# Kernel tuning notes

Hardware: AMD Instinct MI355X
Metric: run time of the kernel (lower is better)

The kernel has to match this reference:

```python
import jax, jax.numpy as jnp
import numpy as np

NUM_GRAPHS = 64
NODE_SZ = 200
FEAT = 200
HID = 256          # hidden_size; each signed branch outputs HID//2
HALF = HID // 2
N_NODES = NUM_GRAPHS * NODE_SZ
N_EDGES = 409600
NUM_LAYERS = 3


def _lin_init(key, out_f, in_f):
    kw, kb = jax.random.split(key)
    s = 1.0 / np.sqrt(in_f)
    W = jax.random.uniform(kw, (out_f, in_f), minval=-s, maxval=s, dtype=jnp.float32)
    b = jax.random.uniform(kb, (out_f,), minval=-s, maxval=s, dtype=jnp.float32)
    return W, b


def setup_inputs() -> dict:
    key = jax.random.key(0)
    ks = jax.random.split(key, 16)
    x = jax.random.normal(ks[0], (N_NODES, FEAT), dtype=jnp.float32)
    edge_index = jax.random.randint(ks[1], (2, N_EDGES), 0, N_NODES, dtype=jnp.int64)
    edge_weight = jax.random.normal(ks[2], (N_EDGES,), dtype=jnp.float32)
    batch = jnp.repeat(jnp.arange(NUM_GRAPHS, dtype=jnp.int64), NODE_SZ)

    # signed conv layer params: layer0 in=FEAT, layers 1..: in=HID; each lin maps 2*in -> HALF
    Wp0, bp0 = _lin_init(ks[3], HALF, 2 * FEAT)
    Wn0, bn0 = _lin_init(ks[4], HALF, 2 * FEAT)
    Wp1, bp1 = _lin_init(ks[5], HALF, 2 * HID)
    Wn1, bn1 = _lin_init(ks[6], HALF, 2 * HID)
    Wp2, bp2 = _lin_init(ks[7], HALF, 2 * HID)
    Wn2, bn2 = _lin_init(ks[8], HALF, 2 * HID)
    Wr, br = _lin_init(ks[9], HID, NODE_SZ * HID)   # readout_lin
    Wl, bl = _lin_init(ks[10], 1, HID)              # final lin
    return dict(x=x, edge_index=edge_index, edge_weight=edge_weight, batch=batch,
                Wp0=Wp0, bp0=bp0, Wn0=Wn0, bn0=bn0,
                Wp1=Wp1, bp1=bp1, Wn1=Wn1, bn1=bn1,
                Wp2=Wp2, bp2=bp2, Wn2=Wn2, bn2=bn2,
                Wr=Wr, br=br, Wl=Wl, bl=bl)


def _signed_conv(x, src, dst, w, Wp, bp, Wn, bn):
    # edge-weighted signed mean aggregation, split by weight sign
    xs = x[src]                                   # [E, D] gather
    pw = jnp.where(w > 0, w, 0.0)
    nw = jnp.where(w < 0, -w, 0.0)
    agg_p = jax.ops.segment_sum(pw[:, None] * xs, dst, num_segments=N_NODES)
    agg_n = jax.ops.segment_sum(nw[:, None] * xs, dst, num_segments=N_NODES)
    deg_p = jax.ops.segment_sum((w > 0).astype(x.dtype), dst, num_segments=N_NODES)
    deg_n = jax.ops.segment_sum((w < 0).astype(x.dtype), dst, num_segments=N_NODES)
    agg_p = agg_p / jnp.maximum(deg_p, 1.0)[:, None]
    agg_n = agg_n / jnp.maximum(deg_n, 1.0)[:, None]
    hp = jnp.concatenate([agg_p, x], -1) @ Wp.T + bp
    hn = jnp.concatenate([agg_n, x], -1) @ Wn.T + bn
    return jnp.concatenate([hp, hn], -1)          # [N, HID]


def reference(x, edge_index, edge_weight, batch,
              Wp0, bp0, Wn0, bn0, Wp1, bp1, Wn1, bn1, Wp2, bp2, Wn2, bn2,
              Wr, br, Wl, bl):
    src, dst = edge_index[0], edge_index[1]
    convs = [(Wp0, bp0, Wn0, bn0), (Wp1, bp1, Wn1, bn1), (Wp2, bp2, Wn2, bn2)]
    h = x
    for i, (Wp, bp, Wn, bn) in enumerate(convs):
        h = _signed_conv(h, src, dst, edge_weight, Wp, bp, Wn, bn)
        if i < NUM_LAYERS - 1:
            h = jax.nn.leaky_relu(h, negative_slope=0.01)
    # per-graph readout: batch is contiguous with NODE_SZ nodes per graph,
    # so the boolean-mask+view loop is exactly a reshape.
    g = h.reshape(NUM_GRAPHS, NODE_SZ * HID)
    g = g @ Wr.T + br                             # [G, HID]
    # dropout(p=0.5) is identity in eval mode
    return g @ Wl.T + bl                          # [G, 1]
```

## Files before the change

### kernel.cpp

```cpp
#include <hip/hip_runtime.h>

#define NUM_GRAPHS 64
#define NODE_SZ    200
#define FEAT       200
#define HID        256
#define HALF       128
#define N_NODES    (NUM_GRAPHS * NODE_SZ)
#define KREAD      (NODE_SZ * HID)
#define HBLK       128

typedef unsigned short ushort_t;
typedef unsigned int uint_t;
typedef __attribute__((ext_vector_type(8))) short bf16x8;
typedef __attribute__((ext_vector_type(4))) float f32x4;

#define GAS(p) ((const __attribute__((address_space(1))) void*)(p))
#define LAS(p) ((__attribute__((address_space(3))) void*)(p))

__device__ __forceinline__ float bf2f(ushort_t u) {
    union { unsigned int i; float f; } v; v.i = ((unsigned int)u) << 16; return v.f;
}
__device__ __forceinline__ ushort_t f2bf(float f) {
    union { float f; unsigned int i; } v; v.f = f;
    unsigned int x = v.i;
    unsigned int r = (x + 0x7fffu + ((x >> 16) & 1u)) >> 16;
    return (ushort_t)r;
}

__global__ __launch_bounds__(1024) void bhist_kernel(const int* __restrict__ ei,
                                                     const float* __restrict__ ew,
                                                     uint_t* __restrict__ bh, int E) {
    __shared__ uint_t h[N_NODES];
    for (int i = threadIdx.x; i < N_NODES; i += 1024) h[i] = 0;
    __syncthreads();
    int b = blockIdx.x;
    int epb = (E + HBLK - 1) / HBLK;
    int e0 = b * epb, e1 = min(e0 + epb, E);
    for (int e = e0 + threadIdx.x; e < e1; e += 1024) {
        int dst = ei[E + e];
        float w = ew[e];
        if (w > 0.0f)      atomicAdd(&h[dst], 1u);
        else if (w < 0.0f) atomicAdd(&h[dst], 0x10000u);
    }
    __syncthreads();
    uint_t* out = bh + (size_t)b * N_NODES;
    for (int i = threadIdx.x * 4; i < N_NODES; i += 4096)
        *(uint4*)&out[i] = *(const uint4*)&h[i];
}

__global__ void colpref_kernel(uint_t* __restrict__ bh, int* __restrict__ counts,
                               int* __restrict__ cnt_p) {
    int n = blockIdx.x * 256 + threadIdx.x;
    if (n >= N_NODES) return;
    uint_t seq = 0;
#pragma unroll 1
    for (int b = 0; b < HBLK; b += 8) {
        uint_t v[8];
#pragma unroll
        for (int j = 0; j < 8; ++j) v[j] = bh[(size_t)(b + j) * N_NODES + n];
#pragma unroll
        for (int j = 0; j < 8; ++j) {
            bh[(size_t)(b + j) * N_NODES + n] = seq;
            seq += v[j];
        }
    }
    counts[n] = (int)((seq & 0xffffu) + (seq >> 16));
    cnt_p[n]  = (int)(seq & 0xffffu);
}

__global__ __launch_bounds__(1024) void scan_kernel(const int* __restrict__ counts,
                                                    const int* __restrict__ cnt_p,
                                                    uint2* __restrict__ obnd, int n) {
    const int PER = 13;
    int t = threadIdx.x;
    int start = t * PER;
    int local[PER];
    int sum = 0;
#pragma unroll
    for (int i = 0; i < PER; ++i) {
        int idx = start + i;
        int v = (idx < n) ? counts[idx] : 0;
        local[i] = sum;
        sum += v;
    }
    int lane = t & 63, wid = t >> 6;
    int inc = sum;
#pragma unroll
    for (int d = 1; d < 64; d <<= 1) {
        int up = __shfl_up(inc, d);
        if (lane >= d) inc += up;
    }
    __shared__ int wsum[16], woff[16];
    if (lane == 63) wsum[wid] = inc;
    __syncthreads();
    if (t < 16) {
        int acc = 0;
        for (int j = 0; j < 16; ++j) if (j < t) acc += wsum[j];
        woff[t] = acc;
    }
    __syncthreads();
    int base = woff[wid] + (inc - sum);
#pragma unroll
    for (int i = 0; i < PER; ++i) {
        int idx = start + i;
        if (idx < n) {
            uint_t off = (uint_t)(base + local[i]);
            obnd[idx] = make_uint2(off, off + (uint_t)cnt_p[idx]);
        }
    }
    if (t == 1023) {
        uint_t tot = (uint_t)(base + sum);
        obnd[n] = make_uint2(tot, tot);
    }
}

__global__ __launch_bounds__(1024) void scat_prep_kernel(
        const int* __restrict__ ei, const float* __restrict__ ew,
        const uint_t* __restrict__ bh, const uint2* __restrict__ obnd,
        uint2* __restrict__ es, int E,
        const float* __restrict__ W0p, const float* __restrict__ W0n,
        const float* __restrict__ W1p, const float* __restrict__ W1n,
        const float* __restrict__ W2p, const float* __restrict__ W2n,
        const float* __restrict__ x,
        ushort_t* __restrict__ wall, ushort_t* __restrict__ xb) {
    __shared__ uint_t cur[N_NODES];
    int bx = blockIdx.x;
    if (bx < HBLK) {
        const uint_t* pref = bh + (size_t)bx * N_NODES;
        for (int i = threadIdx.x * 4; i < N_NODES; i += 4096)
            *(uint4*)&cur[i] = *(const uint4*)&pref[i];
        __syncthreads();
        int epb = (E + HBLK - 1) / HBLK;
        int e0 = bx * epb, e1 = min(e0 + epb, E);
        for (int e = e0 + threadIdx.x; e < e1; e += 1024) {
            int src = ei[e];
            int dst = ei[E + e];
            float w = ew[e];
            if (w > 0.0f) {
                uint_t old = atomicAdd(&cur[dst], 1u);
                uint_t pos = obnd[dst].x + (old & 0xffffu);
                es[pos] = make_uint2((uint_t)src, __float_as_uint(w));
            } else if (w < 0.0f) {
                uint_t old = atomicAdd(&cur[dst], 0x10000u);
                uint_t pos = obnd[dst].y + (old >> 16);
                es[pos] = make_uint2((uint_t)src, __float_as_uint(-w));
            }
        }
    } else if (bx < 512) {
        int idx = (bx - 128) * 1024 + threadIdx.x;
        int layer = idx >> 17;
        int within = idx & 131071;
        int rr = within >> 8;
        int col = within & 255;
        const float* Wp = (layer == 0) ? W0p : (layer == 1) ? W1p : W2p;
        const float* Wn = (layer == 0) ? W0n : (layer == 1) ? W1n : W2n;
        int Ks = (layer == 0) ? 200 : 256;
        int q = rr >> 7;
        const float* Wsrc = (q & 1) ? Wn : Wp;
        int row = rr & 127;
        int scol = col + ((q >> 1) ? Ks : 0);
        float v = (col < Ks) ? Wsrc[(size_t)row * (2 * Ks) + scol] : 0.0f;
        wall[idx] = f2bf(v);
    } else {
        int idx = (bx - 512) * 1024 + threadIdx.x;
        int n = idx >> 6;
        int c0 = (idx & 63) * 4;
        ushort4 o = {0, 0, 0, 0};
        if (c0 < 200) {
            float4 v = *(const float4*)&x[(size_t)n * 200 + c0];
            o.x = f2bf(v.x); o.y = f2bf(v.y); o.z = f2bf(v.z); o.w = f2bf(v.w);
        }
        *(ushort4*)&xb[(size_t)n * 256 + c0] = o;
    }
}

template <int KSTEPS>
__global__ __launch_bounds__(256) void gemm_mfma(
        const ushort_t* __restrict__ A,
        const ushort_t* __restrict__ B,
        ushort_t* __restrict__ Y) {
    __shared__ __align__(16) ushort_t As[2][32 * 32];
    __shared__ __align__(16) ushort_t Bs[2][128 * 32];
    int mBase = blockIdx.x * 32;
    int nBase = blockIdx.y * 128;
    int tid  = threadIdx.x;
    int lane = tid & 63;
    int wv   = tid >> 6;
    int r    = lane & 15;
    int quad = lane >> 4;

    int rowA = tid >> 2, colA = (tid & 3) * 8;
    const ushort_t* gA  = A + (size_t)(mBase + (rowA & 31)) * 256 + colA;
    const ushort_t* gB0 = B + (size_t)(nBase + rowA) * 256 + colA;
    const ushort_t* gB1 = B + (size_t)(nBase + rowA + 64) * 256 + colA;

    f32x4 acc00 = {0.f,0.f,0.f,0.f}, acc01 = {0.f,0.f,0.f,0.f};
    f32x4 acc10 = {0.f,0.f,0.f,0.f}, acc11 = {0.f,0.f,0.f,0.f};

    if (tid < 128)
        __builtin_amdgcn_global_load_lds(GAS(gA), LAS(&As[0][wv * 512]), 16, 0, 0);
    __builtin_amdgcn_global_load_lds(GAS(gB0), LAS(&Bs[0][wv * 512]), 16, 0, 0);
    __builtin_amdgcn_global_load_lds(GAS(gB1), LAS(&Bs[0][2048 + wv * 512]), 16, 0, 0);

    for (int kt = 0; kt < KSTEPS; ++kt) {
        int cur = kt & 1;
        __syncthreads();
        if (kt + 1 < KSTEPS) {
            int kB = (kt + 1) * 32;
            if (tid < 128)
                __builtin_amdgcn_global_load_lds(GAS(gA + kB), LAS(&As[cur ^ 1][wv * 512]), 16, 0, 0);
            __builtin_amdgcn_global_load_lds(GAS(gB0 + kB), LAS(&Bs[cur ^ 1][wv * 512]), 16, 0, 0);
            __builtin_amdgcn_global_load_lds(GAS(gB1 + kB), LAS(&Bs[cur ^ 1][2048 + wv * 512]), 16, 0, 0);
        }
        bf16x8 a0 = *(const bf16x8*)&As[cur][r * 32 + quad * 8];
        bf16x8 a1 = *(const bf16x8*)&As[cur][(16 + r) * 32 + quad * 8];
        bf16x8 b0 = *(const bf16x8*)&Bs[cur][(wv * 32 + r) * 32 + quad * 8];
        bf16x8 b1 = *(const bf16x8*)&Bs[cur][(wv * 32 + 16 + r) * 32 + quad * 8];
        acc00 = __builtin_amdgcn_mfma_f32_16x16x32_bf16(a0, b0, acc00, 0, 0, 0);
        acc01 = __builtin_amdgcn_mfma_f32_16x16x32_bf16(a0, b1, acc01, 0, 0, 0);
        acc10 = __builtin_amdgcn_mfma_f32_16x16x32_bf16(a1, b0, acc10, 0, 0, 0);
        acc11 = __builtin_amdgcn_mfma_f32_16x16x32_bf16(a1, b1, acc11, 0, 0, 0);
    }
#pragma unroll
    for (int jn = 0; jn < 2; ++jn) {
        int cl = nBase + wv * 32 + jn * 16 + r;
        f32x4 am0 = jn ? acc01 : acc00;
        f32x4 am1 = jn ? acc11 : acc10;
#pragma unroll
        for (int reg = 0; reg < 4; ++reg) {
            int m0 = mBase + quad * 4 + reg;
            Y[(size_t)m0 * 512 + cl]        = f2bf(am0[reg]);
            Y[(size_t)(m0 + 16) * 512 + cl] = f2bf(am1[reg]);
        }
    }
}

template <bool LEAKY>
__global__ __launch_bounds__(256) void aggcomb_kernel(
        const ushort_t* __restrict__ Y,
        const uint2* __restrict__ obnd,
        const uint2* __restrict__ es,
        const float* __restrict__ bp, const float* __restrict__ bn,
        ushort_t* __restrict__ out) {
    int lane = threadIdx.x & 63;
    int wv   = threadIdx.x >> 6;
    int n = blockIdx.x * 4 + wv;
    int c0 = lane * 2;
    uint2 ob = obnd[n];
    uint_t off = ob.x, mid = ob.y, end = obnd[n + 1].x;

    float accp[2] = {0.f, 0.f};
    float accn[2] = {0.f, 0.f};

#pragma unroll 1
    for (int phase = 0; phase < 2; ++phase) {
        uint_t lo = phase ? mid : off;
        uint_t hi = phase ? end : mid;
        float* acc = phase ? accn : accp;
        const ushort_t* Yb = Y + (phase ? 128 : 0) + c0;
#pragma unroll 1
        for (uint_t base = lo; base < hi; base += 64) {
            int cnt = (int)min(64u, hi - base);
            uint2 rec = es[base + (uint_t)min(lane, cnt - 1)];
            int i = 0;
#pragma unroll 1
            for (; i + 8 <= cnt; i += 8) {
                int s[8]; float w[8]; uint_t u[8];
#pragma unroll
                for (int j = 0; j < 8; ++j) {
                    s[j] = __shfl((int)rec.x, i + j);
                    w[j] = __uint_as_float((uint_t)__shfl((int)rec.y, i + j));
                }
#pragma unroll
                for (int j = 0; j < 8; ++j) u[j] = *(const uint_t*)&Yb[(size_t)s[j] * 512];
#pragma unroll
                for (int j = 0; j < 8; ++j) {
                    acc[0] = fmaf(w[j], bf2f((ushort_t)(u[j] & 0xffffu)), acc[0]);
                    acc[1] = fmaf(w[j], bf2f((ushort_t)(u[j] >> 16)), acc[1]);
                }
            }
#pragma unroll 1
            for (; i < cnt; ++i) {
                int s = __shfl((int)rec.x, i);
                float w = __uint_as_float((uint_t)__shfl((int)rec.y, i));
                uint_t u = *(const uint_t*)&Yb[(size_t)s * 512];
                acc[0] = fmaf(w, bf2f((ushort_t)(u & 0xffffu)), acc[0]);
                acc[1] = fmaf(w, bf2f((ushort_t)(u >> 16)), acc[1]);
            }
        }
    }

    float dp = fmaxf((float)(mid - off), 1.0f);
    float dn = fmaxf((float)(end - mid), 1.0f);
    float rp = 1.0f / dp, rn = 1.0f / dn;
    uint_t zp = *(const uint_t*)&Y[(size_t)n * 512 + 256 + c0];
    uint_t zn = *(const uint_t*)&Y[(size_t)n * 512 + 384 + c0];
    float vp0 = fmaf(accp[0], rp, bf2f((ushort_t)(zp & 0xffffu)) + bp[c0]);
    float vp1 = fmaf(accp[1], rp, bf2f((ushort_t)(zp >> 16))     + bp[c0 + 1]);
    float vn0 = fmaf(accn[0], rn, bf2f((ushort_t)(zn & 0xffffu)) + bn[c0]);
    float vn1 = fmaf(accn[1], rn, bf2f((ushort_t)(zn >> 16))     + bn[c0 + 1]);
    if (LEAKY) {
        vp0 = (vp0 > 0.0f) ? vp0 : 0.01f * vp0;
        vp1 = (vp1 > 0.0f) ? vp1 : 0.01f * vp1;
        vn0 = (vn0 > 0.0f) ? vn0 : 0.01f * vn0;
        vn1 = (vn1 > 0.0f) ? vn1 : 0.01f * vn1;
    }
    uint_t op = (uint_t)f2bf(vp0) | ((uint_t)f2bf(vp1) << 16);
    uint_t on = (uint_t)f2bf(vn0) | ((uint_t)f2bf(vn1) << 16);
    *(uint_t*)&out[(size_t)n * 256 + c0]       = op;
    *(uint_t*)&out[(size_t)n * 256 + 128 + c0] = on;
}

__global__ __launch_bounds__(256) void readout_mfma(
        const ushort_t* __restrict__ h, const float* __restrict__ Wr,
        float* __restrict__ partial) {
    __shared__ __align__(16) ushort_t As[64 * 32];
    __shared__ __align__(16) ushort_t Bs[64 * 32];
    int nBase  = blockIdx.x * 64;
    int kStart = blockIdx.y * 800;
    int tid  = threadIdx.x;
    int lane = tid & 63;
    int wv   = tid >> 6;
    int r    = lane & 15;
    int quad = lane >> 4;

    f32x4 acc[4];
#pragma unroll
    for (int j = 0; j < 4; ++j) acc[j] = (f32x4){0.f, 0.f, 0.f, 0.f};

    for (int kt = 0; kt < 25; ++kt) {
        int kBase = kStart + kt * 32;
        int lin = tid * 8;
        int row = lin >> 5, col = lin & 31;
        *(uint4*)&As[lin] = *(const uint4*)&h[(size_t)row * KREAD + kBase + col];
        {
            const float* wp = &Wr[(size_t)(nBase + row) * KREAD + kBase + col];
            float4 f0 = *(const float4*)&wp[0];
            float4 f1 = *(const float4*)&wp[4];
            ushort4 b0, b1;
            b0.x = f2bf(f0.x); b0.y = f2bf(f0.y); b0.z = f2bf(f0.z); b0.w = f2bf(f0.w);
            b1.x = f2bf(f1.x); b1.y = f2bf(f1.y); b1.z = f2bf(f1.z); b1.w = f2bf(f1.w);
            *(ushort4*)&Bs[lin]     = b0;
            *(ushort4*)&Bs[lin + 4] = b1;
        }
        __syncthreads();
        bf16x8 a = *(const bf16x8*)&As[(wv * 16 + r) * 32 + quad * 8];
#pragma unroll
        for (int j = 0; j < 4; ++j) {
            bf16x8 b = *(const bf16x8*)&Bs[(j * 16 + r) * 32 + quad * 8];
            acc[j] = __builtin_amdgcn_mfma_f32_16x16x32_bf16(a, b, acc[j], 0, 0, 0);
        }
        __syncthreads();
    }
    float* out = partial + (size_t)blockIdx.y * (64 * HID);
#pragma unroll
    for (int j = 0; j < 4; ++j) {
        int c = nBase + j * 16 + r;
#pragma unroll
        for (int reg = 0; reg < 4; ++reg) {
            int g = wv * 16 + quad * 4 + reg;
            out[g * HID + c] = acc[j][reg];
        }
    }
}

__global__ void final_kernel(const float* __restrict__ partial, const float* __restrict__ br,
                             const float* __restrict__ Wl, const float* __restrict__ bl,
                             float* __restrict__ out) {
    int g = blockIdx.x;
    int c = threadIdx.x;
    float s = 0.0f;
#pragma unroll 4
    for (int k = 0; k < 64; ++k) s += partial[(size_t)k * (64 * HID) + g * HID + c];
    float v = (s + br[c]) * Wl[c];
#pragma unroll
    for (int d = 32; d > 0; d >>= 1) v += __shfl_down(v, d);
    __shared__ float sh[4];
    if ((c & 63) == 0) sh[c >> 6] = v;
    __syncthreads();
    if (c == 0) out[g] = sh[0] + sh[1] + sh[2] + sh[3] + bl[0];
}

extern "C" void kernel_launch(void* const* d_in, const int* in_sizes, int n_in,
                              void* d_out, int out_size, void* d_ws, size_t ws_size,
                              hipStream_t stream) {
    const float* x  = (const float*)d_in[0];
    const int*   ei = (const int*)d_in[1];
    const float* ew = (const float*)d_in[2];
    const float* Wp0 = (const float*)d_in[4];
    const float* bp0 = (const float*)d_in[5];
    const float* Wn0 = (const float*)d_in[6];
    const float* bn0 = (const float*)d_in[7];
    const float* Wp1 = (const float*)d_in[8];
    const float* bp1 = (const float*)d_in[9];
    const float* Wn1 = (const float*)d_in[10];
    const float* bn1 = (const float*)d_in[11];
    const float* Wp2 = (const float*)d_in[12];
    const float* bp2 = (const float*)d_in[13];
    const float* Wn2 = (const float*)d_in[14];
    const float* bn2 = (const float*)d_in[15];
    const float* Wr  = (const float*)d_in[16];
    const float* br  = (const float*)d_in[17];
    const float* Wl  = (const float*)d_in[18];
    const float* bl  = (const float*)d_in[19];
    const int E = in_sizes[1] / 2;

    char* ws = (char*)d_ws;
    float*    partial = (float*)(ws + 0);
    uint_t*   bh      = (uint_t*)(ws + 4194304);
    int*      counts  = (int*)(ws + 10747904);
    int*      cnt_p   = (int*)(ws + 10799104);
    uint2*    obnd    = (uint2*)(ws + 10850304);
    uint2*    es      = (uint2*)(ws + 10952768);
    ushort_t* Yall    = (ushort_t*)(ws + 14229568);
    ushort_t* hA      = (ushort_t*)(ws + 27336768);
    ushort_t* hB      = (ushort_t*)(ws + 33890368);
    ushort_t* wall    = (ushort_t*)(ws + 40443968);
    ushort_t* xb      = (ushort_t*)(ws + 41230400);

    hipLaunchKernelGGL(bhist_kernel, dim3(HBLK), dim3(1024), 0, stream, ei, ew, bh, E);
    hipLaunchKernelGGL(colpref_kernel, dim3((N_NODES + 255) / 256), dim3(256), 0, stream,
                       bh, counts, cnt_p);
    hipLaunchKernelGGL(scan_kernel, dim3(1), dim3(1024), 0, stream, counts, cnt_p, obnd, N_NODES);
    hipLaunchKernelGGL(scat_prep_kernel, dim3(1312), dim3(1024), 0, stream,
                       ei, ew, bh, obnd, es, E,
                       Wp0, Wn0, Wp1, Wn1, Wp2, Wn2, x, wall, xb);

    hipLaunchKernelGGL((gemm_mfma<7>), dim3(N_NODES / 32, 4), dim3(256), 0, stream,
                       xb, wall + 0 * 131072, Yall);
    hipLaunchKernelGGL((aggcomb_kernel<true>), dim3(N_NODES / 4), dim3(256), 0, stream,
                       Yall, obnd, es, bp0, bn0, hA);
    hipLaunchKernelGGL((gemm_mfma<8>), dim3(N_NODES / 32, 4), dim3(256), 0, stream,
                       hA, wall + 1 * 131072, Yall);
    hipLaunchKernelGGL((aggcomb_kernel<true>), dim3(N_NODES / 4), dim3(256), 0, stream,
                       Yall, obnd, es, bp1, bn1, hB);
    hipLaunchKernelGGL((gemm_mfma<8>), dim3(N_NODES / 32, 4), dim3(256), 0, stream,
                       hB, wall + 2 * 131072, Yall);
    hipLaunchKernelGGL((aggcomb_kernel<false>), dim3(N_NODES / 4), dim3(256), 0, stream,
                       Yall, obnd, es, bp2, bn2, hA);

    hipLaunchKernelGGL(readout_mfma, dim3(4, 64), dim3(256), 0, stream, hA, Wr, partial);
    hipLaunchKernelGGL(final_kernel, dim3(NUM_GRAPHS), dim3(256), 0, stream,
                       partial, br, Wl, bl, (float*)d_out);
}
```

Baseline: 296.8 us.

## Fuse edge scatter with first GEMM, use global-atomic histogram, enlarge GEMM tiles

The per-block LDS histogram, column prefix kernel and large per-block offset buffer are replaced by one global-atomic histogram over packed positive/negative counts, which the scan reads directly. The CSR edge scatter now runs in the same launch as the layer-0 GEMM: the first blocks do the GEMM and the rest place edges. Weight/x conversion and counter zeroing move into a separate prep kernel. The GEMM switches to 128x256 tiles with 512 threads, always doing 8 K-steps. This cuts kernel launches and offset traffic, at the cost of more contention on global atomics and a non-deterministic edge order within each node.

```diff
diff --git a/kernel.cpp b/kernel.cpp
--- a/kernel.cpp
+++ b/kernel.cpp
@@ -7,7 +7,6 @@
 #define HALF       128
 #define N_NODES    (NUM_GRAPHS * NODE_SZ)
 #define KREAD      (NODE_SZ * HID)
-#define HBLK       128
 
 typedef unsigned short ushort_t;
 typedef unsigned int uint_t;
@@ -27,59 +26,66 @@
     return (ushort_t)r;
 }
 
-__global__ __launch_bounds__(1024) void bhist_kernel(const int* __restrict__ ei,
-                                                     const float* __restrict__ ew,
-                                                     uint_t* __restrict__ bh, int E) {
-    __shared__ uint_t h[N_NODES];
-    for (int i = threadIdx.x; i < N_NODES; i += 1024) h[i] = 0;
-    __syncthreads();
-    int b = blockIdx.x;
-    int epb = (E + HBLK - 1) / HBLK;
-    int e0 = b * epb, e1 = min(e0 + epb, E);
-    for (int e = e0 + threadIdx.x; e < e1; e += 1024) {
+__global__ __launch_bounds__(256) void prep_kernel(
+        const float* __restrict__ Wp0, const float* __restrict__ Wn0,
+        const float* __restrict__ Wp1, const float* __restrict__ Wn1,
+        const float* __restrict__ Wp2, const float* __restrict__ Wn2,
+        const float* __restrict__ x,
+        uint_t* __restrict__ cntcur, ushort_t* __restrict__ wall,
+        ushort_t* __restrict__ xb) {
+    int gid = blockIdx.x * 256 + threadIdx.x;
+    const int GS = gridDim.x * 256;
+    for (int i = gid; i < 2 * N_NODES; i += GS) cntcur[i] = 0u;
+    for (int idx = gid; idx < 3 * 131072; idx += GS) {
+        int layer = idx >> 17, within = idx & 131071;
+        int rr = within >> 8, col = within & 255;
+        const float* Wp = (layer == 0) ? Wp0 : (layer == 1) ? Wp1 : Wp2;
+        const float* Wn = (layer == 0) ? Wn0 : (layer == 1) ? Wn1 : Wn2;
+        int Ks = (layer == 0) ? 200 : 256;
+        int q = rr >> 7;
+        const float* Wsrc = (q & 1) ? Wn : Wp;
+        int row = rr & 127;
+        int scol = col + ((q >> 1) ? Ks : 0);
+        float v = (col < Ks) ? Wsrc[(size_t)row * (2 * Ks) + scol] : 0.0f;
+        wall[idx] = f2bf(v);
+    }
+    for (int idx = gid; idx < N_NODES * 64; idx += GS) {
+        int n = idx >> 6, c0 = (idx & 63) * 4;
+        ushort4 o = {0, 0, 0, 0};
+        if (c0 < 200) {
+            float4 v = *(const float4*)&x[(size_t)n * 200 + c0];
+            o.x = f2bf(v.x); o.y = f2bf(v.y); o.z = f2bf(v.z); o.w = f2bf(v.w);
+        }
+        *(ushort4*)&xb[(size_t)n * 256 + c0] = o;
+    }
+}
+
+__global__ __launch_bounds__(512) void hist_kernel(const int* __restrict__ ei,
+                                                   const float* __restrict__ ew,
+                                                   uint_t* __restrict__ cnt, int E) {
+    int e = blockIdx.x * 512 + threadIdx.x;
+    if (e < E) {
         int dst = ei[E + e];
         float w = ew[e];
-        if (w > 0.0f)      atomicAdd(&h[dst], 1u);
-        else if (w < 0.0f) atomicAdd(&h[dst], 0x10000u);
-    }
-    __syncthreads();
-    uint_t* out = bh + (size_t)b * N_NODES;
-    for (int i = threadIdx.x * 4; i < N_NODES; i += 4096)
-        *(uint4*)&out[i] = *(const uint4*)&h[i];
-}
-
-__global__ void colpref_kernel(uint_t* __restrict__ bh, int* __restrict__ counts,
-                               int* __restrict__ cnt_p) {
-    int n = blockIdx.x * 256 + threadIdx.x;
-    if (n >= N_NODES) return;
-    uint_t seq = 0;
-#pragma unroll 1
-    for (int b = 0; b < HBLK; b += 8) {
-        uint_t v[8];
-#pragma unroll
-        for (int j = 0; j < 8; ++j) v[j] = bh[(size_t)(b + j) * N_NODES + n];
-#pragma unroll
-        for (int j = 0; j < 8; ++j) {
-            bh[(size_t)(b + j) * N_NODES + n] = seq;
-            seq += v[j];
-        }
-    }
-    counts[n] = (int)((seq & 0xffffu) + (seq >> 16));
-    cnt_p[n]  = (int)(seq & 0xffffu);
-}
-
-__global__ __launch_bounds__(1024) void scan_kernel(const int* __restrict__ counts,
-                                                    const int* __restrict__ cnt_p,
+        if (w > 0.0f)      atomicAdd(&cnt[dst], 1u);
+        else if (w < 0.0f) atomicAdd(&cnt[dst], 0x10000u);
+    }
+}
+
+__global__ __launch_bounds__(1024) void scan_kernel(const uint_t* __restrict__ cnt,
                                                     uint2* __restrict__ obnd, int n) {
     const int PER = 13;
     int t = threadIdx.x;
     int start = t * PER;
     int local[PER];
+    uint_t pcnt[PER];
     int sum = 0;
 #pragma unroll
     for (int i = 0; i < PER; ++i) {
         int idx = start + i;
-        int v = (idx < n) ? counts[idx] : 0;
+        uint_t c = (idx < n) ? cnt[idx] : 0u;
+        int v = (int)((c & 0xffffu) + (c >> 16));
+        pcnt[i] = c & 0xffffu;
         local[i] = sum;
         sum += v;
     }
@@ -105,7 +111,7 @@
         int idx = start + i;
         if (idx < n) {
             uint_t off = (uint_t)(base + local[i]);
-            obnd[idx] = make_uint2(off, off + (uint_t)cnt_p[idx]);
+            obnd[idx] = make_uint2(off, off + pcnt[i]);
         }
     }
     if (t == 1023) {
@@ -114,134 +120,111 @@
     }
 }
 
-__global__ __launch_bounds__(1024) void scat_prep_kernel(
-        const int* __restrict__ ei, const float* __restrict__ ew,
-        const uint_t* __restrict__ bh, const uint2* __restrict__ obnd,
-        uint2* __restrict__ es, int E,
-        const float* __restrict__ W0p, const float* __restrict__ W0n,
-        const float* __restrict__ W1p, const float* __restrict__ W1n,
-        const float* __restrict__ W2p, const float* __restrict__ W2n,
-        const float* __restrict__ x,
-        ushort_t* __restrict__ wall, ushort_t* __restrict__ xb) {
-    __shared__ uint_t cur[N_NODES];
-    int bx = blockIdx.x;
-    if (bx < HBLK) {
-        const uint_t* pref = bh + (size_t)bx * N_NODES;
-        for (int i = threadIdx.x * 4; i < N_NODES; i += 4096)
-            *(uint4*)&cur[i] = *(const uint4*)&pref[i];
-        __syncthreads();
-        int epb = (E + HBLK - 1) / HBLK;
-        int e0 = bx * epb, e1 = min(e0 + epb, E);
-        for (int e = e0 + threadIdx.x; e < e1; e += 1024) {
-            int src = ei[e];
-            int dst = ei[E + e];
-            float w = ew[e];
-            if (w > 0.0f) {
-                uint_t old = atomicAdd(&cur[dst], 1u);
-                uint_t pos = obnd[dst].x + (old & 0xffffu);
-                es[pos] = make_uint2((uint_t)src, __float_as_uint(w));
-            } else if (w < 0.0f) {
-                uint_t old = atomicAdd(&cur[dst], 0x10000u);
-                uint_t pos = obnd[dst].y + (old >> 16);
-                es[pos] = make_uint2((uint_t)src, __float_as_uint(-w));
-            }
-        }
-    } else if (bx < 512) {
-        int idx = (bx - 128) * 1024 + threadIdx.x;
-        int layer = idx >> 17;
-        int within = idx & 131071;
-        int rr = within >> 8;
-        int col = within & 255;
-        const float* Wp = (layer == 0) ? W0p : (layer == 1) ? W1p : W2p;
-        const float* Wn = (layer == 0) ? W0n : (layer == 1) ? W1n : W2n;
-        int Ks = (layer == 0) ? 200 : 256;
-        int q = rr >> 7;
-        const float* Wsrc = (q & 1) ? Wn : Wp;
-        int row = rr & 127;
-        int scol = col + ((q >> 1) ? Ks : 0);
-        float v = (col < Ks) ? Wsrc[(size_t)row * (2 * Ks) + scol] : 0.0f;
-        wall[idx] = f2bf(v);
-    } else {
-        int idx = (bx - 512) * 1024 + threadIdx.x;
-        int n = idx >> 6;
-        int c0 = (idx & 63) * 4;
-        ushort4 o = {0, 0, 0, 0};
-        if (c0 < 200) {
-            float4 v = *(const float4*)&x[(size_t)n * 200 + c0];
-            o.x = f2bf(v.x); o.y = f2bf(v.y); o.z = f2bf(v.z); o.w = f2bf(v.w);
-        }
-        *(ushort4*)&xb[(size_t)n * 256 + c0] = o;
-    }
-}
-
-template <int KSTEPS>
-__global__ __launch_bounds__(256) void gemm_mfma(
-        const ushort_t* __restrict__ A,
-        const ushort_t* __restrict__ B,
-        ushort_t* __restrict__ Y) {
-    __shared__ __align__(16) ushort_t As[2][32 * 32];
-    __shared__ __align__(16) ushort_t Bs[2][128 * 32];
-    int mBase = blockIdx.x * 32;
-    int nBase = blockIdx.y * 128;
+__device__ __forceinline__ void gemm_body(int t, const ushort_t* __restrict__ A,
+                                          const ushort_t* __restrict__ Bw,
+                                          ushort_t* __restrict__ Y,
+                                          ushort_t* smem) {
+    int mBase = (t >> 1) * 128;
+    int nBase = (t & 1) * 256;
     int tid  = threadIdx.x;
     int lane = tid & 63;
     int wv   = tid >> 6;
     int r    = lane & 15;
     int quad = lane >> 4;
-
-    int rowA = tid >> 2, colA = (tid & 3) * 8;
-    const ushort_t* gA  = A + (size_t)(mBase + (rowA & 31)) * 256 + colA;
-    const ushort_t* gB0 = B + (size_t)(nBase + rowA) * 256 + colA;
-    const ushort_t* gB1 = B + (size_t)(nBase + rowA + 64) * 256 + colA;
-
-    f32x4 acc00 = {0.f,0.f,0.f,0.f}, acc01 = {0.f,0.f,0.f,0.f};
-    f32x4 acc10 = {0.f,0.f,0.f,0.f}, acc11 = {0.f,0.f,0.f,0.f};
-
-    if (tid < 128)
-        __builtin_amdgcn_global_load_lds(GAS(gA), LAS(&As[0][wv * 512]), 16, 0, 0);
-    __builtin_amdgcn_global_load_lds(GAS(gB0), LAS(&Bs[0][wv * 512]), 16, 0, 0);
-    __builtin_amdgcn_global_load_lds(GAS(gB1), LAS(&Bs[0][2048 + wv * 512]), 16, 0, 0);
-
-    for (int kt = 0; kt < KSTEPS; ++kt) {
-        int cur = kt & 1;
+    int wm   = wv >> 1;
+    int wn   = wv & 1;
+
+    int rowA = tid >> 2, colc = (tid & 3) * 8;
+    const ushort_t* gA  = A  + (size_t)(mBase + rowA) * 256 + colc;
+    const ushort_t* gB0 = Bw + (size_t)(nBase + rowA) * 256 + colc;
+    const ushort_t* gB1 = Bw + (size_t)(nBase + 128 + rowA) * 256 + colc;
+
+    f32x4 acc[2][8];
+#pragma unroll
+    for (int i = 0; i < 2; ++i)
+#pragma unroll
+        for (int j = 0; j < 8; ++j) acc[i][j] = (f32x4){0.f, 0.f, 0.f, 0.f};
+
+    auto STAGE = [&](int buf, int kb) {
+        ushort_t* Ad = smem + (buf << 12) + tid * 8;
+        ushort_t* Bd = smem + 8192 + (buf << 13) + tid * 8;
+        __builtin_amdgcn_global_load_lds(GAS(gA + kb), LAS(Ad), 16, 0, 0);
+        __builtin_amdgcn_global_load_lds(GAS(gB0 + kb), LAS(Bd), 16, 0, 0);
+        __builtin_amdgcn_global_load_lds(GAS(gB1 + kb), LAS(Bd + 4096), 16, 0, 0);
+    };
+
+    STAGE(0, 0);
+    for (int kt = 0; kt < 8; ++kt) {
+        int cb = kt & 1;
         __syncthreads();
-        if (kt + 1 < KSTEPS) {
-            int kB = (kt + 1) * 32;
-            if (tid < 128)
-                __builtin_amdgcn_global_load_lds(GAS(gA + kB), LAS(&As[cur ^ 1][wv * 512]), 16, 0, 0);
-            __builtin_amdgcn_global_load_lds(GAS(gB0 + kB), LAS(&Bs[cur ^ 1][wv * 512]), 16, 0, 0);
-            __builtin_amdgcn_global_load_lds(GAS(gB1 + kB), LAS(&Bs[cur ^ 1][2048 + wv * 512]), 16, 0, 0);
-        }
-        bf16x8 a0 = *(const bf16x8*)&As[cur][r * 32 + quad * 8];
-        bf16x8 a1 = *(const bf16x8*)&As[cur][(16 + r) * 32 + quad * 8];
-        bf16x8 b0 = *(const bf16x8*)&Bs[cur][(wv * 32 + r) * 32 + quad * 8];
-        bf16x8 b1 = *(const bf16x8*)&Bs[cur][(wv * 32 + 16 + r) * 32 + quad * 8];
-        acc00 = __builtin_amdgcn_mfma_f32_16x16x32_bf16(a0, b0, acc00, 0, 0, 0);
-        acc01 = __builtin_amdgcn_mfma_f32_16x16x32_bf16(a0, b1, acc01, 0, 0, 0);
-        acc10 = __builtin_amdgcn_mfma_f32_16x16x32_bf16(a1, b0, acc10, 0, 0, 0);
-        acc11 = __builtin_amdgcn_mfma_f32_16x16x32_bf16(a1, b1, acc11, 0, 0, 0);
-    }
-#pragma unroll
-    for (int jn = 0; jn < 2; ++jn) {
-        int cl = nBase + wv * 32 + jn * 16 + r;
-        f32x4 am0 = jn ? acc01 : acc00;
-        f32x4 am1 = jn ? acc11 : acc10;
-#pragma unroll
-        for (int reg = 0; reg < 4; ++reg) {
-            int m0 = mBase + quad * 4 + reg;
-            Y[(size_t)m0 * 512 + cl]        = f2bf(am0[reg]);
-            Y[(size_t)(m0 + 16) * 512 + cl] = f2bf(am1[reg]);
-        }
-    }
+        if (kt < 7) STAGE(cb ^ 1, (kt + 1) * 32);
+        const ushort_t* Ac = smem + (cb << 12);
+        const ushort_t* Bc = smem + 8192 + (cb << 13);
+        bf16x8 af[2];
+#pragma unroll
+        for (int i = 0; i < 2; ++i)
+            af[i] = *(const bf16x8*)&Ac[(wm * 32 + i * 16 + r) * 32 + quad * 8];
+#pragma unroll
+        for (int j = 0; j < 8; ++j) {
+            bf16x8 bfr = *(const bf16x8*)&Bc[(wn * 128 + j * 16 + r) * 32 + quad * 8];
+            acc[0][j] = __builtin_amdgcn_mfma_f32_16x16x32_bf16(af[0], bfr, acc[0][j], 0, 0, 0);
+            acc[1][j] = __builtin_amdgcn_mfma_f32_16x16x32_bf16(af[1], bfr, acc[1][j], 0, 0, 0);
+        }
+    }
+#pragma unroll
+    for (int i = 0; i < 2; ++i)
+#pragma unroll
+        for (int j = 0; j < 8; ++j) {
+            int c = nBase + wn * 128 + j * 16 + r;
+#pragma unroll
+            for (int reg = 0; reg < 4; ++reg) {
+                int m = mBase + wm * 32 + i * 16 + quad * 4 + reg;
+                Y[(size_t)m * 512 + c] = f2bf(acc[i][j][reg]);
+            }
+        }
+}
+
+__global__ __launch_bounds__(512) void scatgemm_kernel(
+        const int* __restrict__ ei, const float* __restrict__ ew,
+        const uint2* __restrict__ obnd, uint_t* __restrict__ cur,
+        uint2* __restrict__ es, int E,
+        const ushort_t* __restrict__ xb, const ushort_t* __restrict__ wall,
+        ushort_t* __restrict__ Yall) {
+    __shared__ __align__(16) ushort_t smem[24576];
+    int bx = blockIdx.x;
+    if (bx < 200) {
+        gemm_body(bx, xb, wall, Yall, smem);
+        return;
+    }
+    int e = (bx - 200) * 512 + threadIdx.x;
+    if (e < E) {
+        int src = ei[e];
+        int dst = ei[E + e];
+        float w = ew[e];
+        if (w > 0.0f) {
+            uint_t old = atomicAdd(&cur[dst], 1u);
+            es[obnd[dst].x + (old & 0xffffu)] = make_uint2((uint_t)src, __float_as_uint(w));
+        } else if (w < 0.0f) {
+            uint_t old = atomicAdd(&cur[dst], 0x10000u);
+            es[obnd[dst].y + (old >> 16)] = make_uint2((uint_t)src, __float_as_uint(-w));
+        }
+    }
+}
+
+__global__ __launch_bounds__(512) void gemm_kernel(const ushort_t* __restrict__ A,
+                                                   const ushort_t* __restrict__ Bw,
+                                                   ushort_t* __restrict__ Y) {
+    __shared__ __align__(16) ushort_t smem[24576];
+    gemm_body(blockIdx.x, A, Bw, Y, smem);
 }
 
 template <bool LEAKY>
-__global__ __launch_bounds__(256) void aggcomb_kernel(
+__global__ __launch_bounds__(256) void agg_kernel(
         const ushort_t* __restrict__ Y,
         const uint2* __restrict__ obnd,
         const uint2* __restrict__ es,
         const float* __restrict__ bp, const float* __restrict__ bn,
-        ushort_t* __restrict__ out) {
+        ushort_t* __restrict__ outp) {
     int lane = threadIdx.x & 63;
     int wv   = threadIdx.x >> 6;
     int n = blockIdx.x * 4 + wv;
@@ -307,8 +290,8 @@
     }
     uint_t op = (uint_t)f2bf(vp0) | ((uint_t)f2bf(vp1) << 16);
     uint_t on = (uint_t)f2bf(vn0) | ((uint_t)f2bf(vn1) << 16);
-    *(uint_t*)&out[(size_t)n * 256 + c0]       = op;
-    *(uint_t*)&out[(size_t)n * 256 + 128 + c0] = on;
+    *(uint_t*)&outp[(size_t)n * 256 + c0]       = op;
+    *(uint_t*)&outp[(size_t)n * 256 + 128 + c0] = on;
 }
 
 __global__ __launch_bounds__(256) void readout_mfma(
@@ -406,39 +389,31 @@
     const int E = in_sizes[1] / 2;
 
     char* ws = (char*)d_ws;
-    float*    partial = (float*)(ws + 0);
-    uint_t*   bh      = (uint_t*)(ws + 4194304);
-    int*      counts  = (int*)(ws + 10747904);
-    int*      cnt_p   = (int*)(ws + 10799104);
-    uint2*    obnd    = (uint2*)(ws + 10850304);
-    uint2*    es      = (uint2*)(ws + 10952768);
-    ushort_t* Yall    = (ushort_t*)(ws + 14229568);
-    ushort_t* hA      = (ushort_t*)(ws + 27336768);
-    ushort_t* hB      = (ushort_t*)(ws + 33890368);
-    ushort_t* wall    = (ushort_t*)(ws + 40443968);
-    ushort_t* xb      = (ushort_t*)(ws + 41230400);
-
-    hipLaunchKernelGGL(bhist_kernel, dim3(HBLK), dim3(1024), 0, stream, ei, ew, bh, E);
-    hipLaunchKernelGGL(colpref_kernel, dim3((N_NODES + 255) / 256), dim3(256), 0, stream,
-                       bh, counts, cnt_p);
-    hipLaunchKernelGGL(scan_kernel, dim3(1), dim3(1024), 0, stream, counts, cnt_p, obnd, N_NODES);
-    hipLaunchKernelGGL(scat_prep_kernel, dim3(1312), dim3(1024), 0, stream,
-                       ei, ew, bh, obnd, es, E,
-                       Wp0, Wn0, Wp1, Wn1, Wp2, Wn2, x, wall, xb);
-
-    hipLaunchKernelGGL((gemm_mfma<7>), dim3(N_NODES / 32, 4), dim3(256), 0, stream,
-                       xb, wall + 0 * 131072, Yall);
-    hipLaunchKernelGGL((aggcomb_kernel<true>), dim3(N_NODES / 4), dim3(256), 0, stream,
+    float*    partial = (float*)(ws);
+    uint_t*   cnt     = (uint_t*)(ws + 4194304);
+    uint_t*   cur     = (uint_t*)(ws + 4245504);
+    uint2*    obnd    = (uint2*)(ws + 4296704);
+    uint2*    es      = (uint2*)(ws + 4399168);
+    ushort_t* Yall    = (ushort_t*)(ws + 7675968);
+    ushort_t* hA      = (ushort_t*)(ws + 20783168);
+    ushort_t* hB      = (ushort_t*)(ws + 27336768);
+    ushort_t* wall    = (ushort_t*)(ws + 33890368);
+    ushort_t* xb      = (ushort_t*)(ws + 34676800);
+
+    hipLaunchKernelGGL(prep_kernel, dim3(512), dim3(256), 0, stream,
+                       Wp0, Wn0, Wp1, Wn1, Wp2, Wn2, x, cnt, wall, xb);
+    hipLaunchKernelGGL(hist_kernel, dim3((E + 511) / 512), dim3(512), 0, stream, ei, ew, cnt, E);
+    hipLaunchKernelGGL(scan_kernel, dim3(1), dim3(1024), 0, stream, cnt, obnd, N_NODES);
+    hipLaunchKernelGGL(scatgemm_kernel, dim3(200 + (E + 511) / 512), dim3(512), 0, stream,
+                       ei, ew, obnd, cur, es, E, xb, wall, Yall);
+    hipLaunchKernelGGL((agg_kernel<true>), dim3(N_NODES / 4), dim3(256), 0, stream,
                        Yall, obnd, es, bp0, bn0, hA);
-    hipLaunchKernelGGL((gemm_mfma<8>), dim3(N_NODES / 32, 4), dim3(256), 0, stream,
-                       hA, wall + 1 * 131072, Yall);
-    hipLaunchKernelGGL((aggcomb_kernel<true>), dim3(N_NODES / 4), dim3(256), 0, stream,
+    hipLaunchKernelGGL(gemm_kernel, dim3(200), dim3(512), 0, stream, hA, wall + 131072, Yall);
+    hipLaunchKernelGGL((agg_kernel<true>), dim3(N_NODES / 4), dim3(256), 0, stream,
                        Yall, obnd, es, bp1, bn1, hB);
-    hipLaunchKernelGGL((gemm_mfma<8>), dim3(N_NODES / 32, 4), dim3(256), 0, stream,
-                       hB, wall + 2 * 131072, Yall);
-    hipLaunchKernelGGL((aggcomb_kernel<false>), dim3(N_NODES / 4), dim3(256), 0, stream,
+    hipLaunchKernelGGL(gemm_kernel, dim3(200), dim3(512), 0, stream, hB, wall + 262144, Yall);
+    hipLaunchKernelGGL((agg_kernel<false>), dim3(N_NODES / 4), dim3(256), 0, stream,
                        Yall, obnd, es, bp2, bn2, hA);
-
     hipLaunchKernelGGL(readout_mfma, dim3(4, 64), dim3(256), 0, stream, hA, Wr, partial);
     hipLaunchKernelGGL(final_kernel, dim3(NUM_GRAPHS), dim3(256), 0, stream,
                        partial, br, Wl, bl, (float*)d_out);
```

After: 303.7 us. 2.3% more time.
